# Performance work log

Hardware: AMD Instinct MI355X
Metric: run time of the kernel (lower is better)

## Reference

```python
import jax, jax.numpy as jnp
import numpy as np
from jax.experimental.ode import odeint

TOL = 1.0  # ODEBlock default: rtol = atol = tol


def _odefunc(x, t, W1, b1, W2, b2):
    # time-concat MLP: f(x, t) = tanh([x, t] @ W1 + b1) @ W2 + b2
    tcol = jnp.full((x.shape[0], 1), t, dtype=x.dtype)  # [B, 1]
    h = jnp.tanh(jnp.concatenate([x, tcol], axis=1) @ W1 + b1)  # [B, H]
    return h @ W2 + b2  # [B, D]


def setup_inputs() -> dict:
    key = jax.random.key(0)
    k1, k2, k3 = jax.random.split(key, 3)
    B, D, H = 4096, 2048, 2048
    # scale weights so the dynamics stay well-conditioned over t in [0,1]
    x = jax.random.normal(k1, (B, D), dtype=jnp.float32)
    W1 = jax.random.normal(k2, (D + 1, H), dtype=jnp.float32) / np.sqrt(D + 1)
    b1 = jnp.zeros((H,), dtype=jnp.float32)
    W2 = jax.random.normal(k3, (H, D), dtype=jnp.float32) / np.sqrt(H)
    b2 = jnp.zeros((D,), dtype=jnp.float32)
    return {"x": x, "W1": W1, "b1": b1, "W2": W2, "b2": b2}


def reference(x, W1, b1, W2, b2):
    f = lambda y, t: _odefunc(y, t, W1, b1, W2, b2)
    ts = jnp.array([0.0, 1.0], dtype=jnp.float32)
    states = odeint(f, x, ts, rtol=TOL, atol=TOL)  # [2, B, D]
    return states[-1]
```

## Files before the change

### kernel.cpp

```cpp
#include <hip/hip_runtime.h>

typedef unsigned short u16;
typedef __attribute__((ext_vector_type(8))) short short8;
typedef __attribute__((ext_vector_type(4))) float floatx4;

#define BD 4096
#define DD 2048
#define NTOT (BD*DD)
#define MAX_STEPS 3

#define CE0 ((float)(35.0/384.0 - 1951.0/21600.0))
#define CE2 ((float)(500.0/1113.0 - 22642.0/50085.0))
#define CE3 ((float)(125.0/192.0 - 451.0/720.0))
#define CE4 ((float)(-2187.0/6784.0 + 12231.0/42400.0))
#define CE5 ((float)(11.0/84.0 - 649.0/6300.0))
#define CE6 ((float)(-1.0/60.0))

#define CM0 ((float)(6025192743.0/30085553152.0/2.0))
#define CM2 ((float)(51252292925.0/65400821598.0/2.0))
#define CM3 ((float)(-2691868925.0/45128329728.0/2.0))
#define CM4 ((float)(187940372067.0/1594534317056.0/2.0))
#define CM5 ((float)(-1776094331.0/19743644256.0/2.0))
#define CM6 ((float)(11237099.0/235043384.0/2.0))

#define CS0 ((float)(35.0/384.0))
#define CS2 ((float)(500.0/1113.0))
#define CS3 ((float)(125.0/192.0))
#define CS4 ((float)(-2187.0/6784.0))
#define CS5 ((float)(11.0/84.0))

#define B50 ((float)(9017.0/3168.0))
#define B51 ((float)(-355.0/33.0))
#define B52 ((float)(46732.0/5247.0))
#define B53 ((float)(49.0/176.0))
#define B54 ((float)(-5103.0/18656.0))

struct Scal {
  float t, dt, last_t, h0, dt_saved;
  float d0s, d1s, d2s, errs;
  float d0, d1;
  int run_flag, accept_flag, cur;
};

__device__ __forceinline__ u16 f2bf(float x) {
  unsigned int u = __float_as_uint(x);
  u += 0x7FFFu + ((u >> 16) & 1u);
  return (u16)(u >> 16);
}
__device__ __forceinline__ float bf2f(u16 h) {
  return __uint_as_float(((unsigned int)h) << 16);
}
__device__ __forceinline__ void splitw(float v, u16* oh, u16* ol, size_t idx) {
  u16 h = f2bf(v);
  oh[idx] = h;
  ol[idx] = f2bf(v - bf2f(h));
}

__device__ __forceinline__ void gload16(const u16* g, u16* l) {
  __builtin_amdgcn_global_load_lds(
      (const __attribute__((address_space(1))) void*)g,
      (__attribute__((address_space(3))) void*)l, 16, 0, 0);
}

__global__ void transpose_hi(const float* __restrict__ W, u16* __restrict__ th,
                             int K, int N) {
  __shared__ float tile[32][33];
  int k0 = blockIdx.x * 32, n0 = blockIdx.y * 32;
  int tx = threadIdx.x, ty = threadIdx.y;
  #pragma unroll
  for (int j = 0; j < 32; j += 8)
    tile[ty + j][tx] = W[(size_t)(k0 + ty + j) * N + n0 + tx];
  __syncthreads();
  #pragma unroll
  for (int j = 0; j < 32; j += 8) {
    int nn = ty + j, kk = tx;
    th[(size_t)(n0 + nn) * K + k0 + kk] = f2bf(tile[kk][nn]);
  }
}

template <int STAGE>
__global__ __launch_bounds__(256, 2)
void gemm_fused(const u16* __restrict__ Ah, const u16* __restrict__ Al,
                const u16* __restrict__ Bt,
                const float* __restrict__ bias, const float* __restrict__ trow,
                int tmode, float alpha_c,
                float bb0, float bb1, float bb2, float bbv,
                float* __restrict__ YA, float* __restrict__ YB,
                float* __restrict__ F,
                float* __restrict__ K2M, float* __restrict__ K3,
                float* __restrict__ K4,
                u16* __restrict__ oh, u16* __restrict__ ol,
                Scal* __restrict__ s, int flag) {
  if (flag == 1 && !s->run_flag) return;

  __shared__ __attribute__((aligned(16))) u16 lAh[2][64 * 64];
  __shared__ __attribute__((aligned(16))) u16 lAl[2][64 * 64];
  __shared__ __attribute__((aligned(16))) u16 lB[2][128 * 64];

  const int tid = threadIdx.x;
  const int lane = tid & 63;
  const int wave = tid >> 6;

  const int lin = blockIdx.x;
  const int xcd = lin & 7;
  const int slot = lin >> 3;
  const int bm = (xcd * 8 + (slot >> 4)) * 64;
  const int bn = (slot & 15) * 128;

  const int m_w = (wave >> 1) * 32;
  const int n_w = (wave & 1) * 64;
  const int lr = lane & 15;

  const int lrow = lane >> 3;
  const int lcol = (((lane & 7) ^ (lane >> 3)) << 3);
  const int ra = wave * 16;
  const int rb = wave * 32;
  const u16* gAh = Ah + (size_t)(bm + ra + lrow) * DD + lcol;
  const u16* gAl = Al + (size_t)(bm + ra + lrow) * DD + lcol;
  const u16* gB  = Bt + (size_t)(bn + rb + lrow) * DD + lcol;

  floatx4 acc[2][4];
  #pragma unroll
  for (int i = 0; i < 2; ++i)
    #pragma unroll
    for (int j = 0; j < 4; ++j)
      acc[i][j] = (floatx4){0.f, 0.f, 0.f, 0.f};

  auto stage = [&](int k0, int b) {
    #pragma unroll
    for (int t = 0; t < 2; ++t) {
      gload16(gAh + k0 + (size_t)(8 * t) * DD, &lAh[b][(ra + 8 * t) * 64]);
      gload16(gAl + k0 + (size_t)(8 * t) * DD, &lAl[b][(ra + 8 * t) * 64]);
    }
    #pragma unroll
    for (int t = 0; t < 4; ++t)
      gload16(gB + k0 + (size_t)(8 * t) * DD, &lB[b][(rb + 8 * t) * 64]);
  };

  stage(0, 0);
  stage(64, 1);
  asm volatile("s_waitcnt vmcnt(8)" ::: "memory");
  __builtin_amdgcn_sched_barrier(0);
  __builtin_amdgcn_s_barrier();
  __builtin_amdgcn_sched_barrier(0);

  const int NT = DD / 64;
  int bufc = 0;
  for (int t = 0; t < NT; ++t) {
    #pragma unroll
    for (int kk = 0; kk < 2; ++kk) {
      const int cb = kk * 4 + (lane >> 4);
      short8 afh[2], afl[2], bfv[4];
      #pragma unroll
      for (int i = 0; i < 2; ++i) {
        int r = m_w + i * 16 + lr;
        int ar = r * 64 + ((cb ^ (lr & 7)) << 3);
        afh[i] = *(const short8*)&lAh[bufc][ar];
        afl[i] = *(const short8*)&lAl[bufc][ar];
      }
      #pragma unroll
      for (int j = 0; j < 4; ++j) {
        int r = n_w + j * 16 + lr;
        bfv[j] = *(const short8*)&lB[bufc][r * 64 + ((cb ^ (lr & 7)) << 3)];
      }
      #pragma unroll
      for (int i = 0; i < 2; ++i)
        #pragma unroll
        for (int j = 0; j < 4; ++j) {
          acc[i][j] = __builtin_amdgcn_mfma_f32_16x16x32_bf16(afh[i], bfv[j], acc[i][j], 0, 0, 0);
          acc[i][j] = __builtin_amdgcn_mfma_f32_16x16x32_bf16(afl[i], bfv[j], acc[i][j], 0, 0, 0);
        }
    }

    if (t < NT - 1) {
      __builtin_amdgcn_sched_barrier(0);
      __builtin_amdgcn_s_barrier();
      __builtin_amdgcn_sched_barrier(0);
      if (t < NT - 2) {
        stage((t + 2) * 64, bufc);
        asm volatile("s_waitcnt vmcnt(8)" ::: "memory");
      } else {
        asm volatile("s_waitcnt vmcnt(0)" ::: "memory");
      }
      __builtin_amdgcn_sched_barrier(0);
      __builtin_amdgcn_s_barrier();
      __builtin_amdgcn_sched_barrier(0);
      bufc ^= 1;
    }
  }

  const int cur = s->cur;
  const float* Yc = cur ? YB : YA;
  float* NY = cur ? YA : YB;
  const float dt = s->dt;
  float tj = 0.f;
  if (STAGE == 100) tj = (tmode == 0) ? (s->t + dt * alpha_c) : s->h0;

  float err_acc = 0.f;
  const int oq = (lane >> 4) * 4;
  const int oc = lane & 15;
  #pragma unroll
  for (int i = 0; i < 2; ++i)
    #pragma unroll
    for (int j = 0; j < 4; ++j)
      #pragma unroll
      for (int r = 0; r < 4; ++r) {
        int m = bm + m_w + i * 16 + oq + r;
        int n = bn + n_w + j * 16 + oc;
        float v = acc[i][j][r] + bias[n];
        size_t idx = (size_t)m * DD + n;
        if constexpr (STAGE == 100) {
          float h = tanhf(v + tj * trow[n]);
          splitw(h, oh, ol, idx);
        } else if constexpr (STAGE == 0) {
          float fv = F[idx];
          float yv = Yc[idx];
          K2M[idx] = v;
          float ys = yv + dt * (bb0 * fv + bbv * v);
          splitw(ys, oh, ol, idx);
        } else if constexpr (STAGE == 1) {
          float fv = F[idx];
          float yv = Yc[idx];
          float k2v = K2M[idx];
          K3[idx] = v;
          float ys = yv + dt * (bb0 * fv + bb1 * k2v + bbv * v);
          splitw(ys, oh, ol, idx);
        } else if constexpr (STAGE == 2) {
          float fv = F[idx];
          float yv = Yc[idx];
          float k2v = K2M[idx];
          float k3v = K3[idx];
          K4[idx] = v;
          float ys = yv + dt * (bb0 * fv + bb1 * k2v + bb2 * k3v + bbv * v);
          splitw(ys, oh, ol, idx);
        } else if constexpr (STAGE == 3) {
          float fv = F[idx], yv = Yc[idx];
          float k2v = K2M[idx], k3v = K3[idx], k4v = K4[idx];
          K2M[idx] = v;
          float ys = yv + dt * (B50 * fv + B51 * k2v + B52 * k3v + B53 * k4v + B54 * v);
          splitw(ys, oh, ol, idx);
        } else if constexpr (STAGE == 4) {
          float fv = F[idx], yv = Yc[idx];
          float k3v = K3[idx], k4v = K4[idx], k5v = K2M[idx];
          float ny = yv + dt * (CS0 * fv + CS2 * k3v + CS3 * k4v + CS4 * k5v + CS5 * v);
          NY[idx] = ny;
          K3[idx]  = CE0 * fv + CE2 * k3v + CE3 * k4v + CE4 * k5v + CE5 * v;
          K2M[idx] = CM0 * fv + CM2 * k3v + CM3 * k4v + CM4 * k5v + CM5 * v;
          splitw(ny, oh, ol, idx);
        } else if constexpr (STAGE == 5) {
          float Ef = K3[idx] + CE6 * v;
          K3[idx] = Ef;
          K2M[idx] += CM6 * v;
          K4[idx] = v;
          float yv = Yc[idx], nyv = NY[idx];
          float e = dt * Ef;
          float tol = 1.f + fmaxf(fabsf(yv), fabsf(nyv));
          float rr = e / tol;
          err_acc += rr * rr;
        } else if constexpr (STAGE == 10) {
          F[idx] = v;
        } else {
          K4[idx] = v;
        }
      }

  if constexpr (STAGE == 5) {
    __syncthreads();
    float* red = (float*)&lAh[0][0];
    red[tid] = err_acc;
    __syncthreads();
    for (int off = 128; off > 0; off >>= 1) {
      if (tid < off) red[tid] += red[tid + off];
      __syncthreads();
    }
    if (tid == 0) atomicAdd(&s->errs, red[0]);
  }
}

__global__ void k_init_scal(Scal* s) {
  s->t = 0.f; s->dt = 0.f; s->last_t = 0.f; s->h0 = 0.f; s->dt_saved = 1.f;
  s->d0s = 0.f; s->d1s = 0.f; s->d2s = 0.f; s->errs = 0.f;
  s->d0 = 0.f; s->d1 = 0.f;
  s->run_flag = 0; s->accept_flag = 0; s->cur = 0;
}

__global__ void k_init_y(const float* __restrict__ x, float* __restrict__ y,
                         u16* __restrict__ ysh, u16* __restrict__ ysl, int n) {
  for (int i = blockIdx.x * blockDim.x + threadIdx.x; i < n; i += gridDim.x * blockDim.x) {
    float v = x[i];
    y[i] = v;
    splitw(v, ysh, ysl, i);
  }
}

__global__ void k_probe_ys(const float* __restrict__ y, const float* __restrict__ f,
                           u16* __restrict__ ysh, u16* __restrict__ ysl, int n,
                           const Scal* __restrict__ s) {
  float h0 = s->h0;
  for (int i = blockIdx.x * blockDim.x + threadIdx.x; i < n; i += gridDim.x * blockDim.x)
    splitw(y[i] + h0 * f[i], ysh, ysl, i);
}

__global__ void k_prep(float* YA, float* YB, float* __restrict__ F,
                       float* __restrict__ K3p, const float* __restrict__ K4p,
                       float* __restrict__ K2M,
                       u16* __restrict__ ysh, u16* __restrict__ ysl, int n,
                       const Scal* __restrict__ s, int mode) {
  if (mode == 0 && !s->run_flag) return;
  int acc = (mode == 0) ? s->accept_flag : 0;
  int cur = s->cur;
  const float* Yc = cur ? YB : YA;
  const float* Yn = cur ? YA : YB;
  float dtn = s->dt, dts = s->dt_saved;
  for (int i = blockIdx.x * blockDim.x + threadIdx.x; i < n; i += gridDim.x * blockDim.x) {
    float fold = F[i];
    float fnew, ynext;
    if (acc) {
      fnew = K4p[i];
      ynext = Yn[i];
      F[i] = fnew;
      K3p[i] = fold;
      K2M[i] = Yc[i] + dts * K2M[i];
    } else {
      fnew = fold;
      ynext = Yc[i];
    }
    splitw(ynext + dtn * 0.2f * fnew, ysh, ysl, i);
  }
}

__global__ void k_d01(const float* __restrict__ y, const float* __restrict__ f,
                      int n, Scal* s) {
  float a0 = 0.f, a1 = 0.f;
  for (int i = blockIdx.x * blockDim.x + threadIdx.x; i < n; i += gridDim.x * blockDim.x) {
    float yv = y[i], fv = f[i];
    float sc = 1.f + fabsf(yv);
    float t0 = yv / sc, t1 = fv / sc;
    a0 += t0 * t0;
    a1 += t1 * t1;
  }
  __shared__ float r0[256], r1[256];
  int tid = threadIdx.x;
  r0[tid] = a0; r1[tid] = a1;
  __syncthreads();
  for (int off = 128; off > 0; off >>= 1) {
    if (tid < off) { r0[tid] += r0[tid + off]; r1[tid] += r1[tid + off]; }
    __syncthreads();
  }
  if (tid == 0) { atomicAdd(&s->d0s, r0[0]); atomicAdd(&s->d1s, r1[0]); }
}

__global__ void k_h0(Scal* s) {
  float d0 = sqrtf(s->d0s);
  float d1 = sqrtf(s->d1s);
  s->d0 = d0; s->d1 = d1;
  s->h0 = (d0 < 1e-5f || d1 < 1e-5f) ? 1e-6f : 0.01f * d0 / d1;
}

__global__ void k_d2(const float* __restrict__ y, const float* __restrict__ f,
                     const float* __restrict__ f1h, int n, Scal* s) {
  float a = 0.f;
  for (int i = blockIdx.x * blockDim.x + threadIdx.x; i < n; i += gridDim.x * blockDim.x) {
    float v = (f1h[i] - f[i]) / (1.f + fabsf(y[i]));
    a += v * v;
  }
  __shared__ float r0[256];
  int tid = threadIdx.x;
  r0[tid] = a;
  __syncthreads();
  for (int off = 128; off > 0; off >>= 1) {
    if (tid < off) r0[tid] += r0[tid + off];
    __syncthreads();
  }
  if (tid == 0) atomicAdd(&s->d2s, r0[0]);
}

__global__ void k_dt(Scal* s) {
  float d2 = sqrtf(s->d2s) / s->h0;
  float h1 = (s->d1 <= 1e-15f && d2 <= 1e-15f)
                 ? fmaxf(1e-6f, s->h0 * 1e-3f)
                 : powf(0.01f / fmaxf(s->d1, d2), 1.0f / 6.0f);
  s->dt = fminf(100.f * s->h0, h1);
  s->t = 0.f;
  s->last_t = 0.f;
}

__global__ void k_step_begin(Scal* s) {
  s->run_flag = (s->t < 1.0f) && (s->dt > 0.f);
  s->accept_flag = 0;
  s->errs = 0.f;
}

__global__ void k_step_end(Scal* s) {
  if (!s->run_flag) { s->accept_flag = 0; return; }
  float ratio = sqrtf(s->errs / (float)NTOT);
  int acc = (ratio <= 1.0f);
  s->accept_flag = acc;
  float dfactor = (ratio < 1.f) ? 1.f : 0.2f;
  float factor = fminf(10.f, fmaxf(0.9f * powf(ratio, -0.2f), dfactor));
  float ndt = (ratio == 0.f) ? s->dt * 10.f : s->dt * factor;
  if (ndt < 0.f) ndt = 0.f;
  if (acc) { s->dt_saved = s->dt; s->last_t = s->t; s->t = s->t + s->dt; }
  s->dt = ndt;
}

__global__ void k_flip(Scal* s) {
  if (s->accept_flag) s->cur ^= 1;
}

__global__ void k_final(const float* YA, const float* YB,
    const float* __restrict__ f0s, const float* __restrict__ f1s,
    float* out, int n, const Scal* s) {
  int cur = s->cur;
  const float* y1s = cur ? YB : YA;
  const float* y0s = cur ? YA : YB;
  float dt = s->dt_saved;
  float r = (1.0f - s->last_t) / (s->t - s->last_t);
  for (int i = blockIdx.x * blockDim.x + threadIdx.x; i < n; i += gridDim.x * blockDim.x) {
    float y0 = y0s[i], y1 = y1s[i], ym = out[i], f0 = f0s[i], f1 = f1s[i];
    float a = 2.f * dt * (f1 - f0) - 8.f * (y1 + y0) + 16.f * ym;
    float b = dt * (5.f * f0 - 3.f * f1) + 18.f * y0 + 14.f * y1 - 32.f * ym;
    float c = dt * (f1 - 4.f * f0) - 11.f * y0 - 5.f * y1 + 16.f * ym;
    float d = dt * f0;
    out[i] = (((a * r + b) * r + c) * r + d) * r + y0;
  }
}

__global__ void k_debug_ws(float* __restrict__ out, int n, float mb) {
  for (int i = blockIdx.x * blockDim.x + threadIdx.x; i < n; i += gridDim.x * blockDim.x)
    out[i] = mb;
}

extern "C" void kernel_launch(void* const* d_in, const int* in_sizes, int n_in,
                              void* d_out, int out_size, void* d_ws, size_t ws_size,
                              hipStream_t stream) {
  const float* x  = (const float*)d_in[0];
  const float* W1 = (const float*)d_in[1];
  const float* b1 = (const float*)d_in[2];
  const float* W2 = (const float*)d_in[3];
  const float* b2 = (const float*)d_in[4];
  float* out = (float*)d_out;
  const float* w1row = W1 + (size_t)2048 * 2048;

  const size_t SZW = (size_t)2048 * 2048 * 2;
  const size_t SZH = (size_t)NTOT * 2;
  const size_t SZF = (size_t)NTOT * 4;
  const size_t NEED = 1024 + 2 * SZW + 4 * SZH + 5 * SZF;

  if (ws_size < NEED) {
    k_debug_ws<<<2048, 256, 0, stream>>>(out, NTOT, (float)(ws_size >> 20));
    return;
  }

  char* base = (char*)d_ws;
  Scal* s = (Scal*)base;
  size_t o = 1024;
  auto take = [&](size_t bytes) { void* p = base + o; o += bytes; return p; };

  u16* W1T = (u16*)take(SZW); u16* W2T = (u16*)take(SZW);
  u16* YSH = (u16*)take(SZH); u16* YSL = (u16*)take(SZH);
  u16* HH  = (u16*)take(SZH); u16* HL  = (u16*)take(SZH);
  float* YA = (float*)take(SZF); float* YB = (float*)take(SZF);
  float* F  = (float*)take(SZF);
  float* K3 = (float*)take(SZF); float* K4 = (float*)take(SZF);
  float* K2M = out;

  const dim3 GG(1024), GB(256);
  const dim3 EG(2048), EB(256);

  #define G1(tmode, alpha, flag) \
    gemm_fused<100><<<GG, GB, 0, stream>>>(YSH, YSL, W1T, b1, w1row, \
        tmode, alpha, 0.f, 0.f, 0.f, 0.f, \
        YA, YB, F, K2M, K3, K4, HH, HL, s, flag)
  #define G2(st, b0, b1c, b2c, bv, flag) \
    gemm_fused<st><<<GG, GB, 0, stream>>>(HH, HL, W2T, b2, nullptr, \
        0, 0.f, b0, b1c, b2c, bv, \
        YA, YB, F, K2M, K3, K4, YSH, YSL, s, flag)

  transpose_hi<<<dim3(64, 64), dim3(32, 8), 0, stream>>>(W1, W1T, 2048, 2048);
  transpose_hi<<<dim3(64, 64), dim3(32, 8), 0, stream>>>(W2, W2T, 2048, 2048);
  k_init_scal<<<1, 1, 0, stream>>>(s);
  k_init_y<<<EG, EB, 0, stream>>>(x, YA, YSH, YSL, NTOT);

  G1(0, 0.f, 0); G2(10, 0.f, 0.f, 0.f, 0.f, 0);
  k_d01<<<1024, 256, 0, stream>>>(YA, F, NTOT, s);
  k_h0<<<1, 1, 0, stream>>>(s);
  k_probe_ys<<<EG, EB, 0, stream>>>(YA, F, YSH, YSL, NTOT, s);
  G1(1, 0.f, 0); G2(11, 0.f, 0.f, 0.f, 0.f, 0);
  k_d2<<<1024, 256, 0, stream>>>(YA, F, K4, NTOT, s);
  k_dt<<<1, 1, 0, stream>>>(s);
  k_prep<<<EG, EB, 0, stream>>>(YA, YB, F, K3, K4, K2M, YSH, YSL, NTOT, s, 1);

  for (int st = 0; st < MAX_STEPS; ++st) {
    k_step_begin<<<1, 1, 0, stream>>>(s);
    G1(0, 0.2f, 1);
    G2(0, (float)(3.0/40.0), 0.f, 0.f, (float)(9.0/40.0), 1);
    G1(0, 0.3f, 1);
    G2(1, (float)(44.0/45.0), (float)(-56.0/15.0), 0.f, (float)(32.0/9.0), 1);
    G1(0, 0.8f, 1);
    G2(2, (float)(19372.0/6561.0), (float)(-25360.0/2187.0),
       (float)(64448.0/6561.0), (float)(-212.0/729.0), 1);
    G1(0, (float)(8.0/9.0), 1);
    G2(3, 0.f, 0.f, 0.f, 0.f, 1);
    G1(0, 1.f, 1);
    G2(4, 0.f, 0.f, 0.f, 0.f, 1);
    G1(0, 1.f, 1);
    G2(5, 0.f, 0.f, 0.f, 0.f, 1);

    k_step_end<<<1, 1, 0, stream>>>(s);
    k_prep<<<EG, EB, 0, stream>>>(YA, YB, F, K3, K4, K2M, YSH, YSL, NTOT, s, 0);
    k_flip<<<1, 1, 0, stream>>>(s);
  }

  k_final<<<EG, EB, 0, stream>>>(YA, YB, K3, F, out, NTOT, s);

  #undef G1
  #undef G2
}
```

Measured before the change: 2.811 ms.

## Stage GEMM epilogue through LDS for vectorized coalesced global access

```diff
diff --git a/kernel.cpp b/kernel.cpp
--- a/kernel.cpp
+++ b/kernel.cpp
@@ -3,6 +3,7 @@
 typedef unsigned short u16;
 typedef __attribute__((ext_vector_type(8))) short short8;
 typedef __attribute__((ext_vector_type(4))) float floatx4;
+typedef __attribute__((ext_vector_type(4))) unsigned short ushortx4;
 
 #define BD 4096
 #define DD 2048
@@ -54,6 +55,17 @@
   u16 h = f2bf(v);
   oh[idx] = h;
   ol[idx] = f2bf(v - bf2f(h));
+}
+__device__ __forceinline__ void splitw4(floatx4 v, u16* oh, u16* ol, size_t idx) {
+  ushortx4 h, l;
+  #pragma unroll
+  for (int e = 0; e < 4; ++e) {
+    u16 hh = f2bf(v[e]);
+    h[e] = hh;
+    l[e] = f2bf(v[e] - bf2f(hh));
+  }
+  *(ushortx4*)&oh[idx] = h;
+  *(ushortx4*)&ol[idx] = l;
 }
 
 __device__ __forceinline__ void gload16(const u16* g, u16* l) {
@@ -93,9 +105,10 @@
                 Scal* __restrict__ s, int flag) {
   if (flag == 1 && !s->run_flag) return;
 
-  __shared__ __attribute__((aligned(16))) u16 lAh[2][64 * 64];
-  __shared__ __attribute__((aligned(16))) u16 lAl[2][64 * 64];
-  __shared__ __attribute__((aligned(16))) u16 lB[2][128 * 64];
+  __shared__ __attribute__((aligned(16))) u16 raw[2][16384];
+  #define AH_OFF 0
+  #define AL_OFF 4096
+  #define B_OFF  8192
 
   const int tid = threadIdx.x;
   const int lane = tid & 63;
@@ -129,20 +142,18 @@
   auto stage = [&](int k0, int b) {
     #pragma unroll
     for (int t = 0; t < 2; ++t) {
-      gload16(gAh + k0 + (size_t)(8 * t) * DD, &lAh[b][(ra + 8 * t) * 64]);
-      gload16(gAl + k0 + (size_t)(8 * t) * DD, &lAl[b][(ra + 8 * t) * 64]);
+      gload16(gAh + k0 + (size_t)(8 * t) * DD, &raw[b][AH_OFF + (ra + 8 * t) * 64]);
+      gload16(gAl + k0 + (size_t)(8 * t) * DD, &raw[b][AL_OFF + (ra + 8 * t) * 64]);
     }
     #pragma unroll
     for (int t = 0; t < 4; ++t)
-      gload16(gB + k0 + (size_t)(8 * t) * DD, &lB[b][(rb + 8 * t) * 64]);
+      gload16(gB + k0 + (size_t)(8 * t) * DD, &raw[b][B_OFF + (rb + 8 * t) * 64]);
   };
 
   stage(0, 0);
   stage(64, 1);
   asm volatile("s_waitcnt vmcnt(8)" ::: "memory");
-  __builtin_amdgcn_sched_barrier(0);
   __builtin_amdgcn_s_barrier();
-  __builtin_amdgcn_sched_barrier(0);
 
   const int NT = DD / 64;
   int bufc = 0;
@@ -155,13 +166,13 @@
       for (int i = 0; i < 2; ++i) {
         int r = m_w + i * 16 + lr;
         int ar = r * 64 + ((cb ^ (lr & 7)) << 3);
-        afh[i] = *(const short8*)&lAh[bufc][ar];
-        afl[i] = *(const short8*)&lAl[bufc][ar];
+        afh[i] = *(const short8*)&raw[bufc][AH_OFF + ar];
+        afl[i] = *(const short8*)&raw[bufc][AL_OFF + ar];
       }
       #pragma unroll
       for (int j = 0; j < 4; ++j) {
         int r = n_w + j * 16 + lr;
-        bfv[j] = *(const short8*)&lB[bufc][r * 64 + ((cb ^ (lr & 7)) << 3)];
+        bfv[j] = *(const short8*)&raw[bufc][B_OFF + r * 64 + ((cb ^ (lr & 7)) << 3)];
       }
       #pragma unroll
       for (int i = 0; i < 2; ++i)
@@ -173,18 +184,14 @@
     }
 
     if (t < NT - 1) {
-      __builtin_amdgcn_sched_barrier(0);
       __builtin_amdgcn_s_barrier();
-      __builtin_amdgcn_sched_barrier(0);
       if (t < NT - 2) {
         stage((t + 2) * 64, bufc);
         asm volatile("s_waitcnt vmcnt(8)" ::: "memory");
       } else {
         asm volatile("s_waitcnt vmcnt(0)" ::: "memory");
       }
-      __builtin_amdgcn_sched_barrier(0);
       __builtin_amdgcn_s_barrier();
-      __builtin_amdgcn_sched_barrier(0);
       bufc ^= 1;
     }
   }
@@ -196,7 +203,8 @@
   float tj = 0.f;
   if (STAGE == 100) tj = (tmode == 0) ? (s->t + dt * alpha_c) : s->h0;
 
-  float err_acc = 0.f;
+  __syncthreads();
+  float* ep = (float*)&raw[0][0];
   const int oq = (lane >> 4) * 4;
   const int oc = lane & 15;
   #pragma unroll
@@ -204,69 +212,117 @@
     #pragma unroll
     for (int j = 0; j < 4; ++j)
       #pragma unroll
-      for (int r = 0; r < 4; ++r) {
-        int m = bm + m_w + i * 16 + oq + r;
-        int n = bn + n_w + j * 16 + oc;
-        float v = acc[i][j][r] + bias[n];
-        size_t idx = (size_t)m * DD + n;
-        if constexpr (STAGE == 100) {
-          float h = tanhf(v + tj * trow[n]);
-          splitw(h, oh, ol, idx);
-        } else if constexpr (STAGE == 0) {
-          float fv = F[idx];
-          float yv = Yc[idx];
-          K2M[idx] = v;
-          float ys = yv + dt * (bb0 * fv + bbv * v);
-          splitw(ys, oh, ol, idx);
-        } else if constexpr (STAGE == 1) {
-          float fv = F[idx];
-          float yv = Yc[idx];
-          float k2v = K2M[idx];
-          K3[idx] = v;
-          float ys = yv + dt * (bb0 * fv + bb1 * k2v + bbv * v);
-          splitw(ys, oh, ol, idx);
-        } else if constexpr (STAGE == 2) {
-          float fv = F[idx];
-          float yv = Yc[idx];
-          float k2v = K2M[idx];
-          float k3v = K3[idx];
-          K4[idx] = v;
-          float ys = yv + dt * (bb0 * fv + bb1 * k2v + bb2 * k3v + bbv * v);
-          splitw(ys, oh, ol, idx);
-        } else if constexpr (STAGE == 3) {
-          float fv = F[idx], yv = Yc[idx];
-          float k2v = K2M[idx], k3v = K3[idx], k4v = K4[idx];
-          K2M[idx] = v;
-          float ys = yv + dt * (B50 * fv + B51 * k2v + B52 * k3v + B53 * k4v + B54 * v);
-          splitw(ys, oh, ol, idx);
-        } else if constexpr (STAGE == 4) {
-          float fv = F[idx], yv = Yc[idx];
-          float k3v = K3[idx], k4v = K4[idx], k5v = K2M[idx];
-          float ny = yv + dt * (CS0 * fv + CS2 * k3v + CS3 * k4v + CS4 * k5v + CS5 * v);
-          NY[idx] = ny;
-          K3[idx]  = CE0 * fv + CE2 * k3v + CE3 * k4v + CE4 * k5v + CE5 * v;
-          K2M[idx] = CM0 * fv + CM2 * k3v + CM3 * k4v + CM4 * k5v + CM5 * v;
-          splitw(ny, oh, ol, idx);
-        } else if constexpr (STAGE == 5) {
-          float Ef = K3[idx] + CE6 * v;
-          K3[idx] = Ef;
-          K2M[idx] += CM6 * v;
-          K4[idx] = v;
-          float yv = Yc[idx], nyv = NY[idx];
-          float e = dt * Ef;
-          float tol = 1.f + fmaxf(fabsf(yv), fabsf(nyv));
-          float rr = e / tol;
-          err_acc += rr * rr;
-        } else if constexpr (STAGE == 10) {
-          F[idx] = v;
-        } else {
-          K4[idx] = v;
-        }
+      for (int r = 0; r < 4; ++r)
+        ep[(m_w + i * 16 + oq + r) * 132 + (n_w + j * 16 + oc)] = acc[i][j][r];
+  __syncthreads();
+
+  float err_acc = 0.f;
+  #pragma unroll
+  for (int q = 0; q < 8; ++q) {
+    const int fidx = tid + 256 * q;
+    const int rl = fidx >> 5;
+    const int cl = (fidx & 31) << 2;
+    const int n = bn + cl;
+    const size_t idx = (size_t)(bm + rl) * DD + n;
+    floatx4 v = *(const floatx4*)&ep[rl * 132 + cl];
+    {
+      floatx4 b4 = *(const floatx4*)&bias[n];
+      #pragma unroll
+      for (int e = 0; e < 4; ++e) v[e] = v[e] + b4[e];
+    }
+    if constexpr (STAGE == 100) {
+      floatx4 t4 = *(const floatx4*)&trow[n];
+      floatx4 h4;
+      #pragma unroll
+      for (int e = 0; e < 4; ++e) h4[e] = tanhf(v[e] + tj * t4[e]);
+      splitw4(h4, oh, ol, idx);
+    } else if constexpr (STAGE == 0) {
+      floatx4 fv = *(const floatx4*)&F[idx];
+      floatx4 yv = *(const floatx4*)&Yc[idx];
+      *(floatx4*)&K2M[idx] = v;
+      floatx4 ys;
+      #pragma unroll
+      for (int e = 0; e < 4; ++e)
+        ys[e] = yv[e] + dt * (bb0 * fv[e] + bbv * v[e]);
+      splitw4(ys, oh, ol, idx);
+    } else if constexpr (STAGE == 1) {
+      floatx4 fv = *(const floatx4*)&F[idx];
+      floatx4 yv = *(const floatx4*)&Yc[idx];
+      floatx4 k2 = *(const floatx4*)&K2M[idx];
+      *(floatx4*)&K3[idx] = v;
+      floatx4 ys;
+      #pragma unroll
+      for (int e = 0; e < 4; ++e)
+        ys[e] = yv[e] + dt * (bb0 * fv[e] + bb1 * k2[e] + bbv * v[e]);
+      splitw4(ys, oh, ol, idx);
+    } else if constexpr (STAGE == 2) {
+      floatx4 fv = *(const floatx4*)&F[idx];
+      floatx4 yv = *(const floatx4*)&Yc[idx];
+      floatx4 k2 = *(const floatx4*)&K2M[idx];
+      floatx4 k3 = *(const floatx4*)&K3[idx];
+      *(floatx4*)&K4[idx] = v;
+      floatx4 ys;
+      #pragma unroll
+      for (int e = 0; e < 4; ++e)
+        ys[e] = yv[e] + dt * (bb0 * fv[e] + bb1 * k2[e] + bb2 * k3[e] + bbv * v[e]);
+      splitw4(ys, oh, ol, idx);
+    } else if constexpr (STAGE == 3) {
+      floatx4 fv = *(const floatx4*)&F[idx];
+      floatx4 yv = *(const floatx4*)&Yc[idx];
+      floatx4 k2 = *(const floatx4*)&K2M[idx];
+      floatx4 k3 = *(const floatx4*)&K3[idx];
+      floatx4 k4 = *(const floatx4*)&K4[idx];
+      *(floatx4*)&K2M[idx] = v;
+      floatx4 ys;
+      #pragma unroll
+      for (int e = 0; e < 4; ++e)
+        ys[e] = yv[e] + dt * (B50 * fv[e] + B51 * k2[e] + B52 * k3[e] + B53 * k4[e] + B54 * v[e]);
+      splitw4(ys, oh, ol, idx);
+    } else if constexpr (STAGE == 4) {
+      floatx4 fv = *(const floatx4*)&F[idx];
+      floatx4 yv = *(const floatx4*)&Yc[idx];
+      floatx4 k3 = *(const floatx4*)&K3[idx];
+      floatx4 k4 = *(const floatx4*)&K4[idx];
+      floatx4 k5 = *(const floatx4*)&K2M[idx];
+      floatx4 ny, E4, M4;
+      #pragma unroll
+      for (int e = 0; e < 4; ++e) {
+        ny[e] = yv[e] + dt * (CS0 * fv[e] + CS2 * k3[e] + CS3 * k4[e] + CS4 * k5[e] + CS5 * v[e]);
+        E4[e] = CE0 * fv[e] + CE2 * k3[e] + CE3 * k4[e] + CE4 * k5[e] + CE5 * v[e];
+        M4[e] = CM0 * fv[e] + CM2 * k3[e] + CM3 * k4[e] + CM4 * k5[e] + CM5 * v[e];
       }
+      *(floatx4*)&NY[idx] = ny;
+      *(floatx4*)&K3[idx] = E4;
+      *(floatx4*)&K2M[idx] = M4;
+      splitw4(ny, oh, ol, idx);
+    } else if constexpr (STAGE == 5) {
+      floatx4 E4 = *(const floatx4*)&K3[idx];
+      floatx4 M4 = *(const floatx4*)&K2M[idx];
+      floatx4 yv = *(const floatx4*)&Yc[idx];
+      floatx4 nyv = *(const floatx4*)&NY[idx];
+      floatx4 Ef, Mf;
+      #pragma unroll
+      for (int e = 0; e < 4; ++e) {
+        Ef[e] = E4[e] + CE6 * v[e];
+        Mf[e] = M4[e] + CM6 * v[e];
+        float er = dt * Ef[e];
+        float tol = 1.f + fmaxf(fabsf(yv[e]), fabsf(nyv[e]));
+        float rr = er / tol;
+        err_acc += rr * rr;
+      }
+      *(floatx4*)&K3[idx] = Ef;
+      *(floatx4*)&K2M[idx] = Mf;
+      *(floatx4*)&K4[idx] = v;
+    } else if constexpr (STAGE == 10) {
+      *(floatx4*)&F[idx] = v;
+    } else {
+      *(floatx4*)&K4[idx] = v;
+    }
+  }
 
   if constexpr (STAGE == 5) {
     __syncthreads();
-    float* red = (float*)&lAh[0][0];
+    float* red = (float*)&raw[0][0];
     red[tid] = err_acc;
     __syncthreads();
     for (int off = 128; off > 0; off >>= 1) {
```

Result: faster. 2.604 ms (-7.4%).
